# Kernel optimization log

Hardware: AMD Instinct MI355X
Metric: run time of the kernel (lower is better)

The kernel has to match this reference:

```python
import jax, jax.numpy as jnp
import numpy as np

B, N, CA, CS, CZ, H, NQ, NK = 2, 16384, 128, 128, 16, 4, 32, 128
DH = CA // H
NB = N // NQ


def _ln(x, gamma=None, eps=1e-5):
    m = jnp.mean(x, -1, keepdims=True)
    v = jnp.var(x, -1, keepdims=True)
    y = (x - m) * jax.lax.rsqrt(v + eps)
    return y if gamma is None else y * gamma


def _adaln(a, s, gamma_s, Wg, bg, Wskip):
    # AF3 Algorithm 26: LN(a) without affine; LN(s) with scale, no offset;
    # out = sigmoid(Linear(s)) * a + LinearNoBias(s)
    a_n = _ln(a)
    s_n = _ln(s, gamma_s)
    return jax.nn.sigmoid(s_n @ Wg + bg) * a_n + s_n @ Wskip


def setup_inputs():
    key = jax.random.key(0)
    ks = jax.random.split(key, 20)
    def nrm(i, shape, scale=0.02):
        return jax.random.normal(ks[i], shape, jnp.float32) * scale
    return {
        "a": jax.random.normal(ks[0], (B, N, CA), jnp.float32),
        "s": jax.random.normal(ks[1], (B, N, CS), jnp.float32),
        "z": jax.random.normal(ks[2], (B, NB, NQ, NK, CZ), jnp.float32),
        "apb_gamma_s": jnp.ones((CS,), jnp.float32),
        "apb_Wg": nrm(3, (CS, CA)),
        "apb_bg": jnp.zeros((CA,), jnp.float32),
        "apb_Wskip": nrm(4, (CS, CA)),
        "Wq": nrm(5, (CA, CA)), "bq": jnp.zeros((CA,), jnp.float32),
        "Wk": nrm(6, (CA, CA)), "Wv": nrm(7, (CA, CA)),
        "Wgate": nrm(8, (CA, CA)), "Wo": nrm(9, (CA, CA)),
        "gamma_z": jnp.ones((CZ,), jnp.float32),
        "Wz": nrm(10, (CZ, H)),
        "Ws_last": nrm(11, (CS, CA)),
        "bs_last": jnp.full((CA,), -2.0, jnp.float32),
        "ct_gamma_s": jnp.ones((CS,), jnp.float32),
        "ct_Wg": nrm(12, (CS, CA)), "ct_bg": jnp.zeros((CA,), jnp.float32),
        "ct_Wskip": nrm(13, (CS, CA)),
        "Wa1": nrm(14, (CA, 2 * CA)), "Wa2": nrm(15, (CA, 2 * CA)),
        "Wb": nrm(16, (2 * CA, CA)),
        "Ws": nrm(17, (CS, CA)), "bs": jnp.full((CA,), -2.0, jnp.float32),
        "n_queries": NQ, "n_keys": NK,
    }


def reference(a, s, z, apb_gamma_s, apb_Wg, apb_bg, apb_Wskip, Wq, bq, Wk, Wv,
              Wgate, Wo, gamma_z, Wz, Ws_last, bs_last, ct_gamma_s, ct_Wg,
              ct_bg, ct_Wskip, Wa1, Wa2, Wb, Ws, bs, n_queries, n_keys):
    nq, nk = int(n_queries), int(n_keys)
    nb = N // nq
    # ---- AttentionPairBias, local windowed attention ----
    a1 = _adaln(a, s, apb_gamma_s, apb_Wg, apb_bg, apb_Wskip)  # [B,N,CA]
    # trunked pair bias: [B,nb,nq,nk,H] -> [B,H,nb,nq,nk]
    bias = jnp.transpose(_ln(z, gamma_z) @ Wz, (0, 4, 1, 2, 3))
    q = (a1 @ Wq + bq).reshape(B, N, H, DH).transpose(0, 2, 1, 3)
    k = (a1 @ Wk).reshape(B, N, H, DH).transpose(0, 2, 1, 3)
    v = (a1 @ Wv).reshape(B, N, H, DH).transpose(0, 2, 1, 3)
    qb = q.reshape(B, H, nb, nq, DH)
    pad = (nk - nq) // 2
    # centered key window per query block
    idx = (jnp.arange(nb) * nq - pad)[:, None] + jnp.arange(nk)[None, :]  # [nb,nk]
    valid = (idx >= 0) & (idx < N)
    idxc = jnp.clip(idx, 0, N - 1)
    kb = k[:, :, idxc]  # [B,H,nb,nk,DH]
    vb = v[:, :, idxc]
    scores = jnp.einsum('bhnqd,bhnkd->bhnqk', qb, kb) / np.sqrt(DH).astype(np.float32) + bias
    scores = jnp.where(valid[None, None, :, None, :], scores, -1e9)
    attn = jax.nn.softmax(scores, axis=-1)
    o = jnp.einsum('bhnqk,bhnkd->bhnqd', attn, vb)  # [B,H,nb,nq,DH]
    o = o.reshape(B, H, N, DH).transpose(0, 2, 1, 3).reshape(B, N, CA)
    g = jax.nn.sigmoid(a1 @ Wgate)  # per-channel gating
    attn_out = (g * o) @ Wo
    b_out = jax.nn.sigmoid(s @ Ws_last + bs_last) * attn_out
    # ---- ConditionedTransitionBlock (Alg 25) ----
    a3 = _adaln(a, s, ct_gamma_s, ct_Wg, ct_bg, ct_Wskip)
    t = jax.nn.silu(a3 @ Wa1) * (a3 @ Wa2)
    ct_out = jax.nn.sigmoid(s @ Ws + bs) * (t @ Wb)
    # Alg 23: a = b + ConditionedTransitionBlock(a, s)
    return b_out + ct_out
```

## Files before the change

### kernel.cpp

```cpp
#include <hip/hip_runtime.h>

typedef _Float16 f16;
typedef f16 f16x8 __attribute__((ext_vector_type(8)));
typedef f16 f16x4 __attribute__((ext_vector_type(4)));
typedef f16 f16x2 __attribute__((ext_vector_type(2)));
typedef float f32x4 __attribute__((ext_vector_type(4)));

#define MFMA16(a,b,c) __builtin_amdgcn_mfma_f32_16x16x32_f16((a),(b),(c),0,0,0)

static __device__ __forceinline__ f16x8 ld8(const f16* p){ return *(const f16x8*)p; }
static __device__ __forceinline__ float sigm(float x){ return 1.f/(1.f + __expf(-x)); }

__global__ __launch_bounds__(256) void k_prep(
    const float* __restrict__ apb_gamma, const float* __restrict__ apb_Wg, const float* __restrict__ apb_Wskip,
    const float* __restrict__ ct_gamma,  const float* __restrict__ ct_Wg,  const float* __restrict__ ct_Wskip,
    const float* __restrict__ Wq, const float* __restrict__ Wk, const float* __restrict__ Wv, const float* __restrict__ Wgate,
    const float* __restrict__ Wsl, const float* __restrict__ Wss,
    const float* __restrict__ Wa1, const float* __restrict__ Wa2,
    const float* __restrict__ Wo, const float* __restrict__ Wb,
    const float* __restrict__ gamma_z, const float* __restrict__ Wz,
    f16* __restrict__ wA, f16* __restrict__ wC, f16* __restrict__ wQK, f16* __restrict__ wVG,
    f16* __restrict__ wSG, f16* __restrict__ wAB, f16* __restrict__ wO, f16* __restrict__ wBt,
    float* __restrict__ wzg, float* __restrict__ Slv, float* __restrict__ Ssv,
    float* __restrict__ wcs)
{
  const int t0 = blockIdx.x*256 + threadIdx.x;
  const int stride = gridDim.x*256;
  for (int i = t0; i < 256*128; i += stride){
    const int n = i >> 7, k = i & 127;
    const int m = n & 127;
    wA[i]  = (f16)(((n<128) ? apb_Wg[k*128+m] : apb_Wskip[k*128+m]) * apb_gamma[k]);
    wC[i]  = (f16)(((n<128) ? ct_Wg[k*128+m]  : ct_Wskip[k*128+m])  * ct_gamma[k]);
    wQK[i] = (f16)((n<128) ? Wq[k*128+m] : Wk[k*128+m]);
    wVG[i] = (f16)((n<128) ? Wv[k*128+m] : Wgate[k*128+m]);
    wSG[i] = (f16)((n<128) ? Wsl[k*128+m] : Wss[k*128+m]);
  }
  for (int i = t0; i < 512*128; i += stride){
    const int n = i >> 7, k = i & 127;
    wAB[i] = (f16)((n < 256) ? Wa1[k*256 + n] : Wa2[k*256 + (n-256)]);
  }
  for (int i = t0; i < 128*128; i += stride){
    const int n = i >> 7, k = i & 127;
    wO[i] = (f16)Wo[k*128+n];
  }
  for (int i = t0; i < 128*256; i += stride){
    const int n = i >> 8, k = i & 255;
    wBt[i] = (f16)Wb[k*128+n];
  }
  if (t0 < 64) wzg[t0] = gamma_z[t0 & 15] * Wz[(t0 & 15)*4 + (t0 >> 4)];
  if (t0 < 256){
    const int cc = t0 & 127;
    const float* Wp = (t0 >= 128) ? Wss : Wsl;
    float acc = 0.f;
    for (int k = 0; k < 128; k++) acc += Wp[k*128 + cc];
    if (t0 >= 128) Ssv[cc] = acc; else Slv[cc] = acc;
  }
  if (t0 < 4){
    float acc = 0.f;
    for (int cc = 0; cc < 16; cc++) acc += gamma_z[cc]*Wz[cc*4 + t0];
    wcs[t0] = acc;
  }
}

__global__ __launch_bounds__(256,3) void k_pre(
    const float* __restrict__ A, const float* __restrict__ S,
    const f16* __restrict__ wA, const f16* __restrict__ wC,
    const f16* __restrict__ wQK, const f16* __restrict__ wVG,
    const f16* __restrict__ wSG, const f16* __restrict__ wAB,
    const float* __restrict__ bgA, const float* __restrict__ bgC,
    const float* __restrict__ bq, const float* __restrict__ bsl, const float* __restrict__ bss,
    const float* __restrict__ Slv, const float* __restrict__ Ssv,
    f16* __restrict__ Qo, f16* __restrict__ Ko, f16* __restrict__ Vt, f16* __restrict__ Go,
    f16* __restrict__ T, f16* __restrict__ GL, f16* __restrict__ GS)
{
  __shared__ __attribute__((aligned(16))) f16 lsn[64*136];
  __shared__ __attribute__((aligned(16))) f16 lan[64*136];
  __shared__ __attribute__((aligned(16))) f16 la1[64*136];
  __shared__ float lsm[64], lsd[64];
  const int tid = threadIdx.x;
  const size_t rbase = (size_t)blockIdx.x * 64;

  {
    const int row = tid >> 2, part = tid & 3;
    const size_t gr = rbase + row;
    {
      const float* sp = S + gr*128 + part*32;
      float v[32];
      #pragma unroll
      for (int j = 0; j < 8; j++){
        const float4 t4 = ((const float4*)sp)[j];
        v[j*4+0]=t4.x; v[j*4+1]=t4.y; v[j*4+2]=t4.z; v[j*4+3]=t4.w;
      }
      float sm = 0.f, sq = 0.f;
      #pragma unroll
      for (int j = 0; j < 32; j++){ sm += v[j]; sq += v[j]*v[j]; }
      sm += __shfl_xor(sm,1); sq += __shfl_xor(sq,1);
      sm += __shfl_xor(sm,2); sq += __shfl_xor(sq,2);
      const float mean = sm*(1.f/128.f);
      const float var  = sq*(1.f/128.f) - mean*mean;
      const float rstd = rsqrtf(var + 1e-5f);
      if (part == 0){ lsm[row] = mean; lsd[row] = (var + 1e-5f)*rstd; }
      #pragma unroll
      for (int j = 0; j < 4; j++){
        f16x8 o;
        #pragma unroll
        for (int e = 0; e < 8; e++) o[e] = (f16)((v[j*8+e]-mean)*rstd);
        *(f16x8*)&lsn[row*136 + part*32 + j*8] = o;
      }
    }
    {
      const float* ap = A + gr*128 + part*32;
      float v[32];
      #pragma unroll
      for (int j = 0; j < 8; j++){
        const float4 t4 = ((const float4*)ap)[j];
        v[j*4+0]=t4.x; v[j*4+1]=t4.y; v[j*4+2]=t4.z; v[j*4+3]=t4.w;
      }
      float sm = 0.f, sq = 0.f;
      #pragma unroll
      for (int j = 0; j < 32; j++){ sm += v[j]; sq += v[j]*v[j]; }
      sm += __shfl_xor(sm,1); sq += __shfl_xor(sq,1);
      sm += __shfl_xor(sm,2); sq += __shfl_xor(sq,2);
      const float mean = sm*(1.f/128.f);
      const float var  = sq*(1.f/128.f) - mean*mean;
      const float rstd = rsqrtf(var + 1e-5f);
      #pragma unroll
      for (int j = 0; j < 4; j++){
        f16x8 o;
        #pragma unroll
        for (int e = 0; e < 8; e++) o[e] = (f16)((v[j*8+e]-mean)*rstd);
        *(f16x8*)&lan[row*136 + part*32 + j*8] = o;
      }
    }
  }
  __syncthreads();

  const int l = tid & 63, w = tid >> 6;
  const int c = l & 15, q4 = l >> 4;

  for (int jj = 0; jj < 2; jj++){
    const int n0 = (jj*4 + w)*16;
    const float bvA = bgA[n0 + c], bvC = bgC[n0 + c];
    f16x8 bA0[4], bA1[4], bC0[4], bC1[4];
    #pragma unroll
    for (int kc = 0; kc < 4; kc++){
      bA0[kc] = ld8(wA + (size_t)(n0 + c)*128 + kc*32 + q4*8);
      bA1[kc] = ld8(wA + (size_t)(128 + n0 + c)*128 + kc*32 + q4*8);
      bC0[kc] = ld8(wC + (size_t)(n0 + c)*128 + kc*32 + q4*8);
      bC1[kc] = ld8(wC + (size_t)(128 + n0 + c)*128 + kc*32 + q4*8);
    }
    for (int mi = 0; mi < 4; mi++){
      f32x4 dA0 = {0,0,0,0}, dA1 = {0,0,0,0}, dC0 = {0,0,0,0}, dC1 = {0,0,0,0};
      #pragma unroll
      for (int kc = 0; kc < 4; kc++){
        const f16x8 av = *(const f16x8*)&lsn[(mi*16 + c)*136 + kc*32 + q4*8];
        dA0 = MFMA16(av, bA0[kc], dA0);
        dA1 = MFMA16(av, bA1[kc], dA1);
        dC0 = MFMA16(av, bC0[kc], dC0);
        dC1 = MFMA16(av, bC1[kc], dC1);
      }
      #pragma unroll
      for (int r = 0; r < 4; r++){
        const int row = mi*16 + q4*4 + r;
        const float anv = (float)lan[row*136 + n0 + c];
        la1[row*136 + n0 + c] = (f16)(sigm(dA0[r] + bvA)*anv + dA1[r]);
        lan[row*136 + n0 + c] = (f16)(sigm(dC0[r] + bvC)*anv + dC1[r]);
      }
    }
  }
  __syncthreads();

  for (int jj = 0; jj < 2; jj++){
    const int n0 = (jj*4 + w)*16;
    f16x8 bQ[4], bK[4], bV[4], bG[4];
    #pragma unroll
    for (int kc = 0; kc < 4; kc++){
      bQ[kc] = ld8(wQK + (size_t)(n0 + c)*128 + kc*32 + q4*8);
      bK[kc] = ld8(wQK + (size_t)(128 + n0 + c)*128 + kc*32 + q4*8);
      bV[kc] = ld8(wVG + (size_t)(n0 + c)*128 + kc*32 + q4*8);
      bG[kc] = ld8(wVG + (size_t)(128 + n0 + c)*128 + kc*32 + q4*8);
    }
    const float bvq = bq[n0 + c];
    for (int mi = 0; mi < 4; mi++){
      f32x4 dQ = {0,0,0,0}, dK = {0,0,0,0}, dV = {0,0,0,0}, dG = {0,0,0,0};
      #pragma unroll
      for (int kc = 0; kc < 4; kc++){
        const f16x8 av = *(const f16x8*)&la1[(mi*16 + c)*136 + kc*32 + q4*8];
        dQ = MFMA16(av, bQ[kc], dQ);
        dK = MFMA16(av, bK[kc], dK);
        dV = MFMA16(av, bV[kc], dV);
        dG = MFMA16(av, bG[kc], dG);
      }
      #pragma unroll
      for (int r = 0; r < 4; r++){
        const size_t grow = rbase + mi*16 + q4*4 + r;
        Qo[grow*128 + n0 + c] = (f16)((dQ[r] + bvq)*0.17677669529663687f);
        Ko[grow*128 + n0 + c] = (f16)dK[r];
        Go[grow*128 + n0 + c] = (f16)sigm(dG[r]);
      }
      f16x4 vv;
      #pragma unroll
      for (int r = 0; r < 4; r++) vv[r] = (f16)dV[r];
      const int bidx = (int)(rbase >> 14);
      const int ntk  = (int)(rbase & 16383) + mi*16 + q4*4;
      *(f16x4*)(Vt + ((size_t)bidx*128 + n0 + c)*16384 + ntk) = vv;
    }
  }

  for (int jj = 0; jj < 4; jj++){
    const int n0t = (jj*4 + w)*16;
    f16x8 b1v[4], b2v[4];
    #pragma unroll
    for (int kc = 0; kc < 4; kc++){
      b1v[kc] = ld8(wAB + (size_t)(n0t + c)*128 + kc*32 + q4*8);
      b2v[kc] = ld8(wAB + (size_t)(256 + n0t + c)*128 + kc*32 + q4*8);
    }
    for (int mi = 0; mi < 4; mi++){
      f32x4 d0 = {0,0,0,0}, d1 = {0,0,0,0};
      #pragma unroll
      for (int kc = 0; kc < 4; kc++){
        const f16x8 av = *(const f16x8*)&lan[(mi*16 + c)*136 + kc*32 + q4*8];
        d0 = MFMA16(av, b1v[kc], d0);
        d1 = MFMA16(av, b2v[kc], d1);
      }
      #pragma unroll
      for (int r = 0; r < 4; r++){
        const size_t grow = rbase + mi*16 + q4*4 + r;
        const float u = d0[r];
        T[grow*256 + n0t + c] = (f16)((u*sigm(u))*d1[r]);
      }
    }
  }

  for (int jj = 0; jj < 2; jj++){
    const int n0 = (jj*4 + w)*16;
    f16x8 b0[4], b1[4];
    #pragma unroll
    for (int kc = 0; kc < 4; kc++){
      b0[kc] = ld8(wSG + (size_t)(n0 + c)*128 + kc*32 + q4*8);
      b1[kc] = ld8(wSG + (size_t)(128 + n0 + c)*128 + kc*32 + q4*8);
    }
    const float slc = Slv[n0 + c], ssc = Ssv[n0 + c];
    const float bl = bsl[n0 + c],  bs2 = bss[n0 + c];
    for (int mi = 0; mi < 4; mi++){
      f32x4 d0 = {0,0,0,0}, d1 = {0,0,0,0};
      #pragma unroll
      for (int kc = 0; kc < 4; kc++){
        const f16x8 av = *(const f16x8*)&lsn[(mi*16 + c)*136 + kc*32 + q4*8];
        d0 = MFMA16(av, b0[kc], d0);
        d1 = MFMA16(av, b1[kc], d1);
      }
      #pragma unroll
      for (int r = 0; r < 4; r++){
        const int row = mi*16 + q4*4 + r;
        const size_t grow = rbase + row;
        const float mn = lsm[row], sd = lsd[row];
        GL[grow*128 + n0 + c] = (f16)sigm(d0[r]*sd + mn*slc + bl);
        GS[grow*128 + n0 + c] = (f16)sigm(d1[r]*sd + mn*ssc + bs2);
      }
    }
  }
}

__global__ __launch_bounds__(512,2) void k_attn(const f16* __restrict__ Q, const f16* __restrict__ K,
    const f16* __restrict__ VT, const float* __restrict__ Z, const float* __restrict__ WZG,
    const float* __restrict__ WCS,
    const f16* __restrict__ G, const f16* __restrict__ T,
    const f16* __restrict__ GL, const f16* __restrict__ GS,
    const f16* __restrict__ Wot, const f16* __restrict__ Wbt,
    float* __restrict__ out)
{
  __shared__ __attribute__((aligned(16))) f16 upb[17408];
  __shared__ __attribute__((aligned(16))) f16 obuf[32*136];
  __shared__ float wzg_s[64];
  __shared__ float wcs_s[4];
  const int tid = threadIdx.x;
  const int b = blockIdx.x >> 9, nb = blockIdx.x & 511;
  if (tid < 64) wzg_s[tid] = WZG[tid];
  if (tid < 4)  wcs_s[tid] = WCS[tid];

  const int l = tid & 63, w = tid >> 6;
  const int c = l & 15, q4 = l >> 4;
  const int h = w >> 1, qh = w & 1, m0 = qh*16;

  const f16x8 aq = ld8(Q + ((size_t)b*16384 + (size_t)nb*32 + m0 + c)*128 + h*32 + q4*8);
  const long kbase = (long)b*16384 + (long)nb*32 - 48;
  f32x4 sc[8];
  #pragma unroll
  for (int nt = 0; nt < 8; nt++){
    const f16x8 bf = ld8(K + (kbase + nt*16 + c)*128 + h*32 + q4*8);
    f32x4 zz = {0.f,0.f,0.f,0.f};
    sc[nt] = MFMA16(aq, bf, zz);
  }

  __syncthreads();
  #pragma unroll
  for (int i = 0; i < 8; i++){
    const int p  = tid + i*512;
    const int qq = p >> 7, kk = p & 127;
    const float* zp = Z + ((((size_t)b*512 + nb)*32 + qq)*128 + kk)*16;
    const float4 z0 = *(const float4*)(zp);
    const float4 z1 = *(const float4*)(zp + 4);
    const float4 z2 = *(const float4*)(zp + 8);
    const float4 z3 = *(const float4*)(zp + 12);
    const float xs[16] = {z0.x,z0.y,z0.z,z0.w, z1.x,z1.y,z1.z,z1.w,
                          z2.x,z2.y,z2.z,z2.w, z3.x,z3.y,z3.z,z3.w};
    float sm = 0.f, sq = 0.f;
    #pragma unroll
    for (int cc = 0; cc < 16; cc++){ sm += xs[cc]; sq += xs[cc]*xs[cc]; }
    const float mean = sm*(1.f/16.f);
    const float var  = sq*(1.f/16.f) - mean*mean;
    const float rs   = rsqrtf(var + 1e-5f);
    #pragma unroll
    for (int hh = 0; hh < 4; hh++){
      float acc = 0.f;
      #pragma unroll
      for (int cc = 0; cc < 16; cc++) acc += xs[cc]*wzg_s[hh*16+cc];
      upb[(hh*32 + qq)*132 + kk] = (f16)((acc - mean*wcs_s[hh])*rs);
    }
  }
  __syncthreads();

  #pragma unroll
  for (int nt = 0; nt < 8; nt++){
    const int key = nt*16 + c;
    const long kt = (long)nb*32 - 48 + key;
    const bool inv = (kt < 0) || (kt >= 16384);
    #pragma unroll
    for (int r = 0; r < 4; r++){
      const float v = sc[nt][r] + (float)upb[(h*32 + m0 + q4*4 + r)*132 + key];
      sc[nt][r] = inv ? -1e9f : v;
    }
  }
  #pragma unroll
  for (int r = 0; r < 4; r++){
    float mx = sc[0][r];
    #pragma unroll
    for (int nt = 1; nt < 8; nt++) mx = fmaxf(mx, sc[nt][r]);
    #pragma unroll
    for (int o = 8; o; o >>= 1) mx = fmaxf(mx, __shfl_xor(mx, o));
    float sum = 0.f;
    #pragma unroll
    for (int nt = 0; nt < 8; nt++){ const float e = __expf(sc[nt][r]-mx); sc[nt][r] = e; sum += e; }
    #pragma unroll
    for (int o = 8; o; o >>= 1) sum += __shfl_xor(sum, o);
    const float inv = 1.f/sum;
    #pragma unroll
    for (int nt = 0; nt < 8; nt++) sc[nt][r] *= inv;
  }
  __syncthreads();
  #pragma unroll
  for (int nt = 0; nt < 8; nt++)
    #pragma unroll
    for (int r = 0; r < 4; r++)
      upb[(w*16 + q4*4 + r)*136 + nt*16 + c] = (f16)sc[nt][r];

  const f16* vb = VT + ((long)b*128)*16384 + (long)nb*32 - 48;
  f32x4 o0 = {0.f,0.f,0.f,0.f}, o1 = {0.f,0.f,0.f,0.f};
  #pragma unroll
  for (int kc = 0; kc < 4; kc++){
    const f16x8 pa = *(const f16x8*)&upb[(w*16 + c)*136 + kc*32 + q4*8];
    const f16x8 v0 = ld8(vb + (long)(h*32 + c)*16384 + kc*32 + q4*8);
    const f16x8 v1 = ld8(vb + (long)(h*32 + 16 + c)*16384 + kc*32 + q4*8);
    o0 = MFMA16(pa, v0, o0);
    o1 = MFMA16(pa, v1, o1);
  }
  #pragma unroll
  for (int r = 0; r < 4; r++){
    obuf[(m0 + q4*4 + r)*136 + h*32 + c]      = (f16)o0[r];
    obuf[(m0 + q4*4 + r)*136 + h*32 + 16 + c] = (f16)o1[r];
  }
  __syncthreads();

  const int n0 = w*16;
  f16x8 bo[4];
  #pragma unroll
  for (int kc = 0; kc < 4; kc++) bo[kc] = ld8(Wot + (size_t)(n0 + c)*128 + kc*32 + q4*8);
  const size_t tok0 = (size_t)b*16384 + (size_t)nb*32;
  #pragma unroll
  for (int mt = 0; mt < 2; mt++){
    const size_t arow = tok0 + mt*16 + c;
    f32x4 d1 = {0,0,0,0}, d2 = {0,0,0,0};
    #pragma unroll
    for (int kc = 0; kc < 4; kc++){
      const f16x8 av = ld8(G + arow*128 + kc*32 + q4*8) *
                       *(const f16x8*)&obuf[(mt*16 + c)*136 + kc*32 + q4*8];
      d1 = MFMA16(av, bo[kc], d1);
    }
    #pragma unroll
    for (int kc = 0; kc < 8; kc++){
      const f16x8 at = ld8(T + arow*256 + kc*32 + q4*8);
      d2 = MFMA16(at, ld8(Wbt + (size_t)(n0 + c)*256 + kc*32 + q4*8), d2);
    }
    #pragma unroll
    for (int r = 0; r < 4; r++){
      const size_t row = tok0 + mt*16 + q4*4 + r;
      const float glv = (float)GL[row*128 + n0 + c];
      const float gsv = (float)GS[row*128 + n0 + c];
      out[row*128 + n0 + c] = glv*d1[r] + gsv*d2[r];
    }
  }
}

extern "C" void kernel_launch(void* const* d_in, const int* in_sizes, int n_in,
                              void* d_out, int out_size, void* d_ws, size_t ws_size,
                              hipStream_t stream)
{
  (void)in_sizes; (void)n_in; (void)out_size; (void)ws_size;
  const float* a        = (const float*)d_in[0];
  const float* s        = (const float*)d_in[1];
  const float* z        = (const float*)d_in[2];
  const float* apb_gamma= (const float*)d_in[3];
  const float* apb_Wg   = (const float*)d_in[4];
  const float* apb_bg   = (const float*)d_in[5];
  const float* apb_Wskip= (const float*)d_in[6];
  const float* Wq       = (const float*)d_in[7];
  const float* bq       = (const float*)d_in[8];
  const float* Wk       = (const float*)d_in[9];
  const float* Wv       = (const float*)d_in[10];
  const float* Wgate    = (const float*)d_in[11];
  const float* Wo       = (const float*)d_in[12];
  const float* gamma_z  = (const float*)d_in[13];
  const float* Wz       = (const float*)d_in[14];
  const float* Wsl      = (const float*)d_in[15];
  const float* bsl      = (const float*)d_in[16];
  const float* ct_gamma = (const float*)d_in[17];
  const float* ct_Wg    = (const float*)d_in[18];
  const float* ct_bg    = (const float*)d_in[19];
  const float* ct_Wskip = (const float*)d_in[20];
  const float* Wa1      = (const float*)d_in[21];
  const float* Wa2      = (const float*)d_in[22];
  const float* Wb       = (const float*)d_in[23];
  const float* Wss      = (const float*)d_in[24];
  const float* bss      = (const float*)d_in[25];

  f16* W0 = (f16*)d_ws;
  const size_t SL = (size_t)32768*128;
  f16* qv = W0 + 0*SL;
  f16* kv = W0 + 1*SL;
  f16* vt = W0 + 2*SL;
  f16* gv = W0 + 3*SL;
  f16* tv = W0 + 4*SL;
  f16* gl = W0 + 6*SL;
  f16* gs = W0 + 7*SL;
  f16* wA  = W0 + 8*SL;
  f16* wC  = wA  + 256*128;
  f16* wQK = wC  + 256*128;
  f16* wVG = wQK + 256*128;
  f16* wSG = wVG + 256*128;
  f16* wAB = wSG + 256*128;
  f16* wO  = wAB + 512*128;
  f16* wBt = wO  + 128*128;
  float* wzg = (float*)(wBt + 128*256);
  float* Slv = wzg + 64;
  float* Ssv = Slv + 128;
  float* wcs = Ssv + 128;

  k_prep<<<dim3(64),256,0,stream>>>(apb_gamma,apb_Wg,apb_Wskip, ct_gamma,ct_Wg,ct_Wskip,
      Wq,Wk,Wv,Wgate, Wsl,Wss, Wa1,Wa2, Wo,Wb, gamma_z,Wz,
      wA,wC,wQK,wVG,wSG,wAB,wO,wBt,wzg,Slv,Ssv,wcs);
  k_pre<<<dim3(512),256,0,stream>>>(a,s, wA,wC,wQK,wVG,wSG,wAB,
      apb_bg,ct_bg,bq,bsl,bss,Slv,Ssv, qv,kv,vt,gv,tv,gl,gs);
  k_attn<<<dim3(1024),512,0,stream>>>(qv,kv,vt,z,wzg,wcs, gv,tv,gl,gs, wO,wBt,
      (float*)d_out);
}
```

Measured before the change: 581.4 us.

## Split pair-bias computation from z into a separate streaming kernel

Moves the LayerNorm and projection of z into per-head bias out of the attention kernel and into a standalone elementwise kernel that writes an f16 bias tensor, which the attention kernel then loads with vectorized copies. The aim is to take the heavy z streaming (about 268MB of fp32) off the occupancy-limited attention kernel so it runs as a simple, fully parallel bandwidth-bound pass. It also clamps the K and V window indices at the sequence edges so loads stay in bounds. In exchange it adds an extra kernel launch and a round trip of the f16 bias through global memory.

Measured after the change: 568.1 us. -2.3%, faster.

```diff
diff --git a/kernel.cpp b/kernel.cpp
--- a/kernel.cpp
+++ b/kernel.cpp
@@ -62,6 +62,41 @@
   }
 }
 
+__global__ __launch_bounds__(256) void k_zbias(
+    const float* __restrict__ Z, const float* __restrict__ WZG, const float* __restrict__ WCS,
+    f16* __restrict__ Bias)
+{
+  __shared__ float wzg_s[64];
+  __shared__ float wcs_s[4];
+  if (threadIdx.x < 64) wzg_s[threadIdx.x] = WZG[threadIdx.x];
+  if (threadIdx.x < 4)  wcs_s[threadIdx.x] = WCS[threadIdx.x];
+  __syncthreads();
+  const int e = blockIdx.x*256 + threadIdx.x;
+  const int kk  = e & 127;
+  const int qq  = (e >> 7) & 31;
+  const int bnb = e >> 12;
+  const float* zp = Z + (size_t)e*16;
+  const float4 z0 = *(const float4*)(zp);
+  const float4 z1 = *(const float4*)(zp + 4);
+  const float4 z2 = *(const float4*)(zp + 8);
+  const float4 z3 = *(const float4*)(zp + 12);
+  const float xs[16] = {z0.x,z0.y,z0.z,z0.w, z1.x,z1.y,z1.z,z1.w,
+                        z2.x,z2.y,z2.z,z2.w, z3.x,z3.y,z3.z,z3.w};
+  float sm = 0.f, sq = 0.f;
+  #pragma unroll
+  for (int cc = 0; cc < 16; cc++){ sm += xs[cc]; sq += xs[cc]*xs[cc]; }
+  const float mean = sm*(1.f/16.f);
+  const float var  = sq*(1.f/16.f) - mean*mean;
+  const float rs   = rsqrtf(var + 1e-5f);
+  #pragma unroll
+  for (int hh = 0; hh < 4; hh++){
+    float acc = 0.f;
+    #pragma unroll
+    for (int cc = 0; cc < 16; cc++) acc += xs[cc]*wzg_s[hh*16+cc];
+    Bias[((size_t)bnb*4 + hh)*4096 + qq*128 + kk] = (f16)((acc - mean*wcs_s[hh])*rs);
+  }
+}
+
 __global__ __launch_bounds__(256,3) void k_pre(
     const float* __restrict__ A, const float* __restrict__ S,
     const f16* __restrict__ wA, const f16* __restrict__ wC,
@@ -263,8 +298,7 @@
 }
 
 __global__ __launch_bounds__(512,2) void k_attn(const f16* __restrict__ Q, const f16* __restrict__ K,
-    const f16* __restrict__ VT, const float* __restrict__ Z, const float* __restrict__ WZG,
-    const float* __restrict__ WCS,
+    const f16* __restrict__ VT, const f16* __restrict__ Bias,
     const f16* __restrict__ G, const f16* __restrict__ T,
     const f16* __restrict__ GL, const f16* __restrict__ GS,
     const f16* __restrict__ Wot, const f16* __restrict__ Wbt,
@@ -272,51 +306,33 @@
 {
   __shared__ __attribute__((aligned(16))) f16 upb[17408];
   __shared__ __attribute__((aligned(16))) f16 obuf[32*136];
-  __shared__ float wzg_s[64];
-  __shared__ float wcs_s[4];
   const int tid = threadIdx.x;
   const int b = blockIdx.x >> 9, nb = blockIdx.x & 511;
-  if (tid < 64) wzg_s[tid] = WZG[tid];
-  if (tid < 4)  wcs_s[tid] = WCS[tid];
 
   const int l = tid & 63, w = tid >> 6;
   const int c = l & 15, q4 = l >> 4;
   const int h = w >> 1, qh = w & 1, m0 = qh*16;
 
   const f16x8 aq = ld8(Q + ((size_t)b*16384 + (size_t)nb*32 + m0 + c)*128 + h*32 + q4*8);
-  const long kbase = (long)b*16384 + (long)nb*32 - 48;
+  const int wbase = nb*32 - 48;
   f32x4 sc[8];
   #pragma unroll
   for (int nt = 0; nt < 8; nt++){
-    const f16x8 bf = ld8(K + (kbase + nt*16 + c)*128 + h*32 + q4*8);
+    int kt = wbase + nt*16 + c;
+    kt = (kt < 0) ? 0 : ((kt > 16383) ? 16383 : kt);
+    const f16x8 bf = ld8(K + ((size_t)b*16384 + kt)*128 + h*32 + q4*8);
     f32x4 zz = {0.f,0.f,0.f,0.f};
     sc[nt] = MFMA16(aq, bf, zz);
   }
 
-  __syncthreads();
-  #pragma unroll
-  for (int i = 0; i < 8; i++){
-    const int p  = tid + i*512;
-    const int qq = p >> 7, kk = p & 127;
-    const float* zp = Z + ((((size_t)b*512 + nb)*32 + qq)*128 + kk)*16;
-    const float4 z0 = *(const float4*)(zp);
-    const float4 z1 = *(const float4*)(zp + 4);
-    const float4 z2 = *(const float4*)(zp + 8);
-    const float4 z3 = *(const float4*)(zp + 12);
-    const float xs[16] = {z0.x,z0.y,z0.z,z0.w, z1.x,z1.y,z1.z,z1.w,
-                          z2.x,z2.y,z2.z,z2.w, z3.x,z3.y,z3.z,z3.w};
-    float sm = 0.f, sq = 0.f;
-    #pragma unroll
-    for (int cc = 0; cc < 16; cc++){ sm += xs[cc]; sq += xs[cc]*xs[cc]; }
-    const float mean = sm*(1.f/16.f);
-    const float var  = sq*(1.f/16.f) - mean*mean;
-    const float rs   = rsqrtf(var + 1e-5f);
-    #pragma unroll
-    for (int hh = 0; hh < 4; hh++){
-      float acc = 0.f;
-      #pragma unroll
-      for (int cc = 0; cc < 16; cc++) acc += xs[cc]*wzg_s[hh*16+cc];
-      upb[(hh*32 + qq)*132 + kk] = (f16)((acc - mean*wcs_s[hh])*rs);
+  {
+    const f16* bp = Bias + (size_t)blockIdx.x*16384;
+    #pragma unroll
+    for (int i = 0; i < 4; i++){
+      const int idx = tid + i*512;
+      const int hq  = idx >> 4;
+      const int kc8 = idx & 15;
+      *(f16x8*)&upb[hq*136 + kc8*8] = ld8(bp + hq*128 + kc8*8);
     }
   }
   __syncthreads();
@@ -324,11 +340,11 @@
   #pragma unroll
   for (int nt = 0; nt < 8; nt++){
     const int key = nt*16 + c;
-    const long kt = (long)nb*32 - 48 + key;
+    const int kt = wbase + key;
     const bool inv = (kt < 0) || (kt >= 16384);
     #pragma unroll
     for (int r = 0; r < 4; r++){
-      const float v = sc[nt][r] + (float)upb[(h*32 + m0 + q4*4 + r)*132 + key];
+      const float v = sc[nt][r] + (float)upb[(h*32 + m0 + q4*4 + r)*136 + key];
       sc[nt][r] = inv ? -1e9f : v;
     }
   }
@@ -355,13 +371,14 @@
     for (int r = 0; r < 4; r++)
       upb[(w*16 + q4*4 + r)*136 + nt*16 + c] = (f16)sc[nt][r];
 
-  const f16* vb = VT + ((long)b*128)*16384 + (long)nb*32 - 48;
   f32x4 o0 = {0.f,0.f,0.f,0.f}, o1 = {0.f,0.f,0.f,0.f};
   #pragma unroll
   for (int kc = 0; kc < 4; kc++){
+    int t0v = wbase + kc*32 + q4*8;
+    t0v = (t0v < 0) ? 0 : ((t0v > 16376) ? 16376 : t0v);
     const f16x8 pa = *(const f16x8*)&upb[(w*16 + c)*136 + kc*32 + q4*8];
-    const f16x8 v0 = ld8(vb + (long)(h*32 + c)*16384 + kc*32 + q4*8);
-    const f16x8 v1 = ld8(vb + (long)(h*32 + 16 + c)*16384 + kc*32 + q4*8);
+    const f16x8 v0 = ld8(VT + ((size_t)b*128 + h*32 + c)*16384 + t0v);
+    const f16x8 v1 = ld8(VT + ((size_t)b*128 + h*32 + 16 + c)*16384 + t0v);
     o0 = MFMA16(pa, v0, o0);
     o1 = MFMA16(pa, v1, o1);
   }
@@ -443,7 +460,8 @@
   f16* tv = W0 + 4*SL;
   f16* gl = W0 + 6*SL;
   f16* gs = W0 + 7*SL;
-  f16* wA  = W0 + 8*SL;
+  f16* bias = W0 + 8*SL;
+  f16* wA  = W0 + 12*SL;
   f16* wC  = wA  + 256*128;
   f16* wQK = wC  + 256*128;
   f16* wVG = wQK + 256*128;
@@ -459,8 +477,9 @@
   k_prep<<<dim3(64),256,0,stream>>>(apb_gamma,apb_Wg,apb_Wskip, ct_gamma,ct_Wg,ct_Wskip,
       Wq,Wk,Wv,Wgate, Wsl,Wss, Wa1,Wa2, Wo,Wb, gamma_z,Wz,
       wA,wC,wQK,wVG,wSG,wAB,wO,wBt,wzg,Slv,Ssv,wcs);
+  k_zbias<<<dim3(16384),256,0,stream>>>(z,wzg,wcs,bias);
   k_pre<<<dim3(512),256,0,stream>>>(a,s, wA,wC,wQK,wVG,wSG,wAB,
       apb_bg,ct_bg,bq,bsl,bss,Slv,Ssv, qv,kv,vt,gv,tv,gl,gs);
-  k_attn<<<dim3(1024),512,0,stream>>>(qv,kv,vt,z,wzg,wcs, gv,tv,gl,gs, wO,wBt,
+  k_attn<<<dim3(1024),512,0,stream>>>(qv,kv,vt,bias, gv,tv,gl,gs, wO,wBt,
       (float*)d_out);
 }
```
